# Kernel tuning notes

Measured on AMD Instinct MI355X. Metric: run time of the kernel, lower is better.

Reference implementation:

```python
import jax, jax.numpy as jnp
import numpy as np

N_NODES = 100000
N_EDGES = 1200000
N_GRAPHS = 256
D_IN = 8
D_H = 64


def setup_inputs() -> dict:
    key = jax.random.key(0)
    ks = jax.random.split(key, 16)
    x = jax.random.normal(ks[0], (N_NODES, D_IN), dtype=jnp.float32)
    edge_index = jax.random.randint(ks[1], (2, N_EDGES), 0, N_NODES, dtype=jnp.int64)
    batch = jnp.sort(jax.random.randint(ks[2], (N_NODES,), 0, N_GRAPHS, dtype=jnp.int64))

    def lin(k, fan_in, fan_out):
        s = 1.0 / np.sqrt(fan_in)
        return jax.random.uniform(k, (fan_in, fan_out), jnp.float32, -s, s)

    # SAGEConv: lin_l (aggregated neighbors, has bias), lin_r (root, no bias)
    W1l = lin(ks[3], D_IN, D_H); b1 = jnp.zeros((D_H,), jnp.float32); W1r = lin(ks[4], D_IN, D_H)
    W2l = lin(ks[5], D_H, D_H);  b2 = jnp.zeros((D_H,), jnp.float32); W2r = lin(ks[6], D_H, D_H)
    W3l = lin(ks[7], D_H, D_H);  b3 = jnp.zeros((D_H,), jnp.float32); W3r = lin(ks[8], D_H, D_H)
    Wc1 = lin(ks[9], D_H, D_H // 2); bc1 = jnp.zeros((D_H // 2,), jnp.float32)
    Wc2 = lin(ks[10], D_H // 2, 1);  bc2 = jnp.zeros((1,), jnp.float32)
    return dict(x=x, edge_index=edge_index, batch=batch,
                W1l=W1l, b1=b1, W1r=W1r, W2l=W2l, b2=b2, W2r=W2r,
                W3l=W3l, b3=b3, W3r=W3r, Wc1=Wc1, bc1=bc1, Wc2=Wc2, bc2=bc2)


def _sage_conv(x, src, dst, Wl, b, Wr):
    # mean-aggregate messages from source -> target, then two linears
    msg = x[src]                                             # [E, d] gather
    agg = jax.ops.segment_sum(msg, dst, num_segments=N_NODES)
    cnt = jax.ops.segment_sum(jnp.ones((src.shape[0],), x.dtype), dst,
                              num_segments=N_NODES)
    mean = agg / jnp.maximum(cnt, 1.0)[:, None]
    return mean @ Wl + b + x @ Wr


def reference(x, edge_index, batch, W1l, b1, W1r, W2l, b2, W2r,
              W3l, b3, W3r, Wc1, bc1, Wc2, bc2):
    src, dst = edge_index[0], edge_index[1]
    h = jax.nn.relu(_sage_conv(x, src, dst, W1l, b1, W1r))
    h = jax.nn.relu(_sage_conv(h, src, dst, W2l, b2, W2r))
    h = _sage_conv(h, src, dst, W3l, b3, W3r)
    g = jax.ops.segment_sum(h, batch, num_segments=N_GRAPHS)  # global_add_pool
    # dropout is identity in eval mode
    g = jax.nn.relu(g @ Wc1 + bc1)
    return g @ Wc2 + bc2
```

## Files before the change

kernel.cpp:

```cpp
#include <hip/hip_runtime.h>

#define N_NODES 100000
#define N_EDGES 1200000
#define N_GRAPHS 256
#define NBUCK 392
#define EBLK 98
#define EPB 12245
#define DCAP 4608

typedef __attribute__((ext_vector_type(8))) short bf16x8;
typedef __attribute__((ext_vector_type(4))) float f32x4;

__device__ inline unsigned short f2b(float f) {
    union { float f; unsigned u; } c; c.f = f;
    unsigned u = c.u;
    u += 0x7fff + ((u >> 16) & 1);
    return (unsigned short)(u >> 16);
}
__device__ inline float blo(unsigned u) { union { unsigned i; float f; } c; c.i = u << 16; return c.f; }
__device__ inline float bhi(unsigned u) { union { unsigned i; float f; } c; c.i = u & 0xffff0000u; return c.f; }
__device__ inline float b2f(unsigned short h) { union { unsigned i; float f; } c; c.i = ((unsigned)h) << 16; return c.f; }

__global__ __launch_bounds__(256) void bucketA(const int* __restrict__ ei, int* __restrict__ histm) {
    __shared__ int h[NBUCK];
    int k = blockIdx.x, tid = threadIdx.x;
    for (int t = tid; t < NBUCK; t += 256) h[t] = 0;
    __syncthreads();
    int e0 = k * EPB, e1 = min(e0 + EPB, N_EDGES);
    for (int e = e0 + tid; e < e1; e += 256) {
        int dd = ei[N_EDGES + e];
        atomicAdd(&h[dd >> 8], 1);
    }
    __syncthreads();
    for (int t = tid; t < NBUCK; t += 256) histm[t * EBLK + k] = h[t];
}

__global__ __launch_bounds__(512) void bucketB(int* __restrict__ histm, int* __restrict__ bstart) {
    __shared__ int sb[512];
    int tid = threadIdx.x;
    int tot = 0;
    if (tid < NBUCK) {
        for (int k = 0; k < EBLK; k++) tot += histm[tid * EBLK + k];
    }
    sb[tid] = tot;
    __syncthreads();
    int acc = tot;
    for (int off = 1; off < 512; off <<= 1) {
        int v = (tid >= off) ? sb[tid - off] : 0;
        __syncthreads();
        sb[tid] = acc = acc + v;
        __syncthreads();
    }
    int excl = acc - tot;
    if (tid < NBUCK) {
        bstart[tid] = excl;
        int run = excl;
        for (int k = 0; k < EBLK; k++) {
            int v = histm[tid * EBLK + k];
            histm[tid * EBLK + k] = run;
            run += v;
        }
    }
    if (tid == 0) bstart[NBUCK] = N_EDGES;
}

__global__ __launch_bounds__(256) void bucketC(const int* __restrict__ ei, const int* __restrict__ histm,
                                               int* __restrict__ ebuf) {
    __shared__ int cur[NBUCK];
    int k = blockIdx.x, tid = threadIdx.x;
    for (int t = tid; t < NBUCK; t += 256) cur[t] = histm[t * EBLK + k];
    __syncthreads();
    int e0 = k * EPB, e1 = min(e0 + EPB, N_EDGES);
    for (int e = e0 + tid; e < e1; e += 256) {
        int ss = ei[e];
        int dd = ei[N_EDGES + e];
        int pos = atomicAdd(&cur[dd >> 8], 1);
        ebuf[pos] = (ss << 8) | (dd & 255);
    }
}

__global__ __launch_bounds__(256) void bucketD(const int* __restrict__ ebuf, const int* __restrict__ bstart,
                                               int* __restrict__ rowptr, int* __restrict__ esrc) {
    __shared__ int ecache[DCAP];
    __shared__ int stage[DCAP];
    __shared__ int hist[256], off[256];
    int b = blockIdx.x, tid = threadIdx.x;
    int seg0 = bstart[b], seg1 = bstart[b + 1];
    int cnt = seg1 - seg0;
    hist[tid] = 0;
    int lim = min(cnt, DCAP);
    for (int i = tid; i < lim; i += 256) ecache[i] = ebuf[seg0 + i];
    __syncthreads();
    for (int i = tid; i < cnt; i += 256) {
        int p = (i < DCAP) ? ecache[i] : ebuf[seg0 + i];
        atomicAdd(&hist[p & 255], 1);
    }
    __syncthreads();
    int v = hist[tid];
    off[tid] = v;
    __syncthreads();
    int acc = v;
    for (int o = 1; o < 256; o <<= 1) {
        int t = (tid >= o) ? off[tid - o] : 0;
        __syncthreads();
        off[tid] = acc = acc + t;
        __syncthreads();
    }
    int excl = acc - v;
    rowptr[b * 256 + tid] = seg0 + excl;
    off[tid] = excl;
    __syncthreads();
    if (cnt <= DCAP) {
        for (int i = tid; i < cnt; i += 256) {
            int p = ecache[i];
            int pos = atomicAdd(&off[p & 255], 1);
            stage[pos] = (p >> 8) << 7;
        }
        __syncthreads();
        for (int i = tid; i < cnt; i += 256) esrc[seg0 + i] = stage[i];
    } else {
        for (int i = tid; i < cnt; i += 256) {
            int p = (i < DCAP) ? ecache[i] : ebuf[seg0 + i];
            int pos = atomicAdd(&off[p & 255], 1);
            esrc[seg0 + pos] = (p >> 8) << 7;
        }
    }
}

__global__ __launch_bounds__(256) void setup_kernel(const float* __restrict__ x, unsigned short* __restrict__ xb,
                                                    const float* __restrict__ W2l, const float* __restrict__ W2r,
                                                    unsigned short* __restrict__ pw2, float* __restrict__ zbase) {
    int blk = blockIdx.x, tid = threadIdx.x;
    if (blk < 391) {
        int n = blk * 256 + tid;
        if (n < N_NODES) {
            const float4* x4 = (const float4*)x;
            float4 v0 = x4[(size_t)n * 2], v1 = x4[(size_t)n * 2 + 1];
            uint4 p;
            p.x = (unsigned)f2b(v0.x) | ((unsigned)f2b(v0.y) << 16);
            p.y = (unsigned)f2b(v0.z) | ((unsigned)f2b(v0.w) << 16);
            p.z = (unsigned)f2b(v1.x) | ((unsigned)f2b(v1.y) << 16);
            p.w = (unsigned)f2b(v1.z) | ((unsigned)f2b(v1.w) << 16);
            ((uint4*)xb)[n] = p;
        }
    } else if (blk < 423) {
        int r = (blk - 391) * 256 + tid;
        int j = r & 7, lane = (r >> 3) & 63, t = (r >> 9) & 3, s = (r >> 11) & 3;
        int k = s * 32 + (lane >> 4) * 8 + j;
        int n = t * 16 + (lane & 15);
        float v = (k < 64) ? W2l[k * 64 + n] : W2r[(k - 64) * 64 + n];
        pw2[r] = f2b(v);
    } else {
        int i = (blk - 423) * 256 + tid;
        if (i < 33024) zbase[i] = 0.0f;
    }
}

__global__ __launch_bounds__(256) void layer1_fused(const float* __restrict__ x, const unsigned short* __restrict__ xb,
                                                    const int* __restrict__ rowptr, const int* __restrict__ esrc,
                                                    const float* __restrict__ Wl, const float* __restrict__ b,
                                                    const float* __restrict__ Wr, unsigned short* __restrict__ ob) {
    __shared__ float sa[4][8], sx[4][8];
    int tid = threadIdx.x;
    int sub = tid >> 6, lane = tid & 63;
    int grp = lane >> 2, q = lane & 3;
    int n = blockIdx.x * 4 + sub;
    int r0 = __builtin_amdgcn_readfirstlane(rowptr[n]);
    int r1 = __builtin_amdgcn_readfirstlane(rowptr[n + 1]);
    const unsigned* xbu = (const unsigned*)xb;
    float a0 = 0.f, a1 = 0.f;
#pragma unroll
    for (int c = 0; c < 2; c++) {
        int idx = r0 + 16 * c + grp;
        if (idx < r1) {
            unsigned v = xbu[(esrc[idx] >> 5) + q];
            a0 += blo(v); a1 += bhi(v);
        }
    }
    for (int e = r0 + 32; e < r1; e += 16) {
        int idx = e + grp;
        if (idx < r1) {
            unsigned v = xbu[(esrc[idx] >> 5) + q];
            a0 += blo(v); a1 += bhi(v);
        }
    }
#pragma unroll
    for (int m = 4; m <= 32; m <<= 1) {
        a0 += __shfl_xor(a0, m);
        a1 += __shfl_xor(a1, m);
    }
    if (lane < 4) { sa[sub][2 * lane] = a0; sa[sub][2 * lane + 1] = a1; }
    if (lane >= 8 && lane < 16) sx[sub][lane - 8] = x[(size_t)n * 8 + (lane - 8)];
    __syncthreads();
    float invn = 1.0f / fmaxf((float)(r1 - r0), 1.0f);
    float al = 0.f, ar = 0.f;
#pragma unroll
    for (int kk = 0; kk < 8; kk++) {
        al += sa[sub][kk] * Wl[kk * 64 + lane];
        ar += sx[sub][kk] * Wr[kk * 64 + lane];
    }
    ob[(size_t)n * 64 + lane] = f2b(fmaxf(al * invn + b[lane] + ar, 0.0f));
}

__global__ __launch_bounds__(256) void agg_gemm(const unsigned short* __restrict__ hb,
                                                const int* __restrict__ rowptr,
                                                const int* __restrict__ esrc,
                                                const unsigned short* __restrict__ pw,
                                                const float* __restrict__ bias,
                                                unsigned short* __restrict__ outb) {
    __shared__ unsigned short smean[16][64];
    int tid = threadIdx.x;
    int sub = tid >> 6, lane = tid & 63;
    int grp = lane >> 3, q = lane & 7;
    int tile = blockIdx.x;
    const uint4* h16 = (const uint4*)hb;
    for (int i = 0; i < 4; i++) {
        int n = tile * 16 + sub * 4 + i;
        int r0 = __builtin_amdgcn_readfirstlane(rowptr[n]);
        int r1 = __builtin_amdgcn_readfirstlane(rowptr[n + 1]);
        uint4 v[3];
#pragma unroll
        for (int c = 0; c < 3; c++) {
            uint4 vv; vv.x = 0u; vv.y = 0u; vv.z = 0u; vv.w = 0u;
            int idx = r0 + 8 * c + grp;
            if (idx < r1) vv = h16[(esrc[idx] >> 4) + q];
            v[c] = vv;
        }
        float a[8];
#pragma unroll
        for (int j = 0; j < 8; j++) a[j] = 0.f;
#pragma unroll
        for (int c = 0; c < 3; c++) {
            a[0] += blo(v[c].x); a[1] += bhi(v[c].x);
            a[2] += blo(v[c].y); a[3] += bhi(v[c].y);
            a[4] += blo(v[c].z); a[5] += bhi(v[c].z);
            a[6] += blo(v[c].w); a[7] += bhi(v[c].w);
        }
        for (int e = r0 + 24; e < r1; e += 8) {
            int idx = e + grp;
            if (idx < r1) {
                uint4 vv = h16[(esrc[idx] >> 4) + q];
                a[0] += blo(vv.x); a[1] += bhi(vv.x);
                a[2] += blo(vv.y); a[3] += bhi(vv.y);
                a[4] += blo(vv.z); a[5] += bhi(vv.z);
                a[6] += blo(vv.w); a[7] += bhi(vv.w);
            }
        }
#pragma unroll
        for (int j = 0; j < 8; j++) {
            a[j] += __shfl_xor(a[j], 8);
            a[j] += __shfl_xor(a[j], 16);
            a[j] += __shfl_xor(a[j], 32);
        }
        if (grp == 0) {
            float invn = 1.0f / fmaxf((float)(r1 - r0), 1.0f);
#pragma unroll
            for (int j = 0; j < 8; j++) smean[sub * 4 + i][q * 8 + j] = f2b(a[j] * invn);
        }
    }
    __syncthreads();
    int col = lane & 15, quad = lane >> 4;
    int m = tile * 16 + col;
    union U { uint4 u; bf16x8 b; };
    U a0, a1, a2, a3;
    a0.u = *(const uint4*)&smean[col][quad * 8];
    a1.u = *(const uint4*)&smean[col][32 + quad * 8];
    const uint4* srow = (const uint4*)(hb + (size_t)m * 64);
    a2.u = srow[quad];
    a3.u = srow[4 + quad];
    const uint4* pwv = (const uint4*)pw;
    int t = sub;
    U b0, b1, b2, b3;
    b0.u = pwv[(0 * 4 + t) * 64 + lane];
    b1.u = pwv[(1 * 4 + t) * 64 + lane];
    b2.u = pwv[(2 * 4 + t) * 64 + lane];
    b3.u = pwv[(3 * 4 + t) * 64 + lane];
    f32x4 acc = {0.f, 0.f, 0.f, 0.f};
    acc = __builtin_amdgcn_mfma_f32_16x16x32_bf16(a0.b, b0.b, acc, 0, 0, 0);
    acc = __builtin_amdgcn_mfma_f32_16x16x32_bf16(a1.b, b1.b, acc, 0, 0, 0);
    acc = __builtin_amdgcn_mfma_f32_16x16x32_bf16(a2.b, b2.b, acc, 0, 0, 0);
    acc = __builtin_amdgcn_mfma_f32_16x16x32_bf16(a3.b, b3.b, acc, 0, 0, 0);
    float bi = bias[t * 16 + col];
#pragma unroll
    for (int i = 0; i < 4; i++) {
        int node = tile * 16 + quad * 4 + i;
        outb[(size_t)node * 64 + t * 16 + col] = f2b(fmaxf(acc[i] + bi, 0.0f));
    }
}

__global__ __launch_bounds__(256) void aggpool3(const unsigned short* __restrict__ hb,
                                                const int* __restrict__ rowptr,
                                                const int* __restrict__ esrc,
                                                const int* __restrict__ batch, float* __restrict__ A) {
    __shared__ float sa[4][64];
    __shared__ int sbat[4];
    int tid = threadIdx.x;
    int sub = tid >> 6, lane = tid & 63;
    int grp = lane >> 3, q = lane & 7;
    int n = blockIdx.x * 4 + sub;
    int r0 = __builtin_amdgcn_readfirstlane(rowptr[n]);
    int r1 = __builtin_amdgcn_readfirstlane(rowptr[n + 1]);
    const uint4* h16 = (const uint4*)hb;
    uint4 v[3];
#pragma unroll
    for (int c = 0; c < 3; c++) {
        uint4 vv; vv.x = 0u; vv.y = 0u; vv.z = 0u; vv.w = 0u;
        int idx = r0 + 8 * c + grp;
        if (idx < r1) {
            int off = esrc[idx];
            vv = h16[(off >> 4) + q];
        }
        v[c] = vv;
    }
    float a[8];
#pragma unroll
    for (int j = 0; j < 8; j++) a[j] = 0.f;
#pragma unroll
    for (int c = 0; c < 3; c++) {
        a[0] += blo(v[c].x); a[1] += bhi(v[c].x);
        a[2] += blo(v[c].y); a[3] += bhi(v[c].y);
        a[4] += blo(v[c].z); a[5] += bhi(v[c].z);
        a[6] += blo(v[c].w); a[7] += bhi(v[c].w);
    }
    for (int e = r0 + 24; e < r1; e += 8) {
        int idx = e + grp;
        if (idx < r1) {
            int off = esrc[idx];
            uint4 vv = h16[(off >> 4) + q];
            a[0] += blo(vv.x); a[1] += bhi(vv.x);
            a[2] += blo(vv.y); a[3] += bhi(vv.y);
            a[4] += blo(vv.z); a[5] += bhi(vv.z);
            a[6] += blo(vv.w); a[7] += bhi(vv.w);
        }
    }
#pragma unroll
    for (int j = 0; j < 8; j++) {
        a[j] += __shfl_xor(a[j], 8);
        a[j] += __shfl_xor(a[j], 16);
        a[j] += __shfl_xor(a[j], 32);
    }
    if (lane == 0) sbat[sub] = batch[n];
    if (grp == 0) {
        float invn = 1.0f / fmaxf((float)(r1 - r0), 1.0f);
#pragma unroll
        for (int j = 0; j < 8; j++) sa[sub][q * 8 + j] = a[j] * invn;
    }
    __syncthreads();
    if (sub == 0) {
        int b0 = sbat[0], b3v = sbat[3];
        if (b0 == b3v) {
            float s = sa[0][lane] + sa[1][lane] + sa[2][lane] + sa[3][lane];
            atomicAdd(&A[b0 * 64 + lane], s);
        } else {
            float acc = sa[0][lane]; int cur = b0;
#pragma unroll
            for (int i = 1; i < 4; i++) {
                int bi = sbat[i];
                if (bi != cur) { atomicAdd(&A[cur * 64 + lane], acc); cur = bi; acc = 0.f; }
                acc += sa[i][lane];
            }
            atomicAdd(&A[cur * 64 + lane], acc);
        }
    }
}

__global__ __launch_bounds__(256) void poolB_kernel(const unsigned short* __restrict__ hb,
                                                    const int* __restrict__ batch,
                                                    float* __restrict__ B, float* __restrict__ cntf) {
    int d = threadIdx.x & 63;
    int grp = threadIdx.x >> 6;
    int n0 = blockIdx.x * 256;
    int cur = -1; float acc = 0.f; int ac = 0;
    for (int i = grp; i < 256; i += 4) {
        int n = n0 + i;
        if (n >= N_NODES) break;
        int bb = batch[n];
        if (bb != cur) {
            if (cur >= 0) {
                atomicAdd(&B[cur * 64 + d], acc);
                if (d == 0) atomicAdd(&cntf[cur], (float)ac);
            }
            cur = bb; acc = 0.f; ac = 0;
        }
        acc += b2f(hb[(size_t)n * 64 + d]);
        ac++;
    }
    if (cur >= 0) {
        atomicAdd(&B[cur * 64 + d], acc);
        if (d == 0) atomicAdd(&cntf[cur], (float)ac);
    }
}

__global__ __launch_bounds__(256) void head2_kernel(const float* __restrict__ A, const float* __restrict__ B,
                                                    const float* __restrict__ cntf,
                                                    const float* __restrict__ W3l, const float* __restrict__ b3,
                                                    const float* __restrict__ W3r,
                                                    const float* __restrict__ Wc1, const float* __restrict__ bc1,
                                                    const float* __restrict__ Wc2, const float* __restrict__ bc2,
                                                    float* __restrict__ out) {
    __shared__ float sA[4][64], sB[4][64], sh3[4][64];
    int tid = threadIdx.x, sub = tid >> 6, lane = tid & 63;
    int gid = blockIdx.x * 4 + sub;
    sA[sub][lane] = A[gid * 64 + lane];
    sB[sub][lane] = B[gid * 64 + lane];
    float cg = cntf[gid];
    __syncthreads();
    float v = cg * b3[lane];
#pragma unroll 8
    for (int k = 0; k < 64; k++) {
        v += sA[sub][k] * W3l[k * 64 + lane] + sB[sub][k] * W3r[k * 64 + lane];
    }
    sh3[sub][lane] = v;
    __syncthreads();
    int j = lane & 31, kh = lane >> 5;
    float a = 0.f;
#pragma unroll
    for (int kk = 0; kk < 32; kk++) {
        int k = kh * 32 + kk;
        a += sh3[sub][k] * Wc1[k * 32 + j];
    }
    a += __shfl_xor(a, 32);
    float contrib = (lane < 32) ? fmaxf(a + bc1[j], 0.0f) * Wc2[j] : 0.0f;
    contrib += __shfl_xor(contrib, 16);
    contrib += __shfl_xor(contrib, 8);
    contrib += __shfl_xor(contrib, 4);
    contrib += __shfl_xor(contrib, 2);
    contrib += __shfl_xor(contrib, 1);
    if (lane == 0) out[gid] = contrib + bc2[0];
}

extern "C" void kernel_launch(void* const* d_in, const int* in_sizes, int n_in,
                              void* d_out, int out_size, void* d_ws, size_t ws_size,
                              hipStream_t stream) {
    const float* x   = (const float*)d_in[0];
    const int*   ei  = (const int*)d_in[1];
    const int*   bat = (const int*)d_in[2];
    const float* W1l = (const float*)d_in[3];
    const float* b1  = (const float*)d_in[4];
    const float* W1r = (const float*)d_in[5];
    const float* W2l = (const float*)d_in[6];
    const float* b2  = (const float*)d_in[7];
    const float* W2r = (const float*)d_in[8];
    const float* W3l = (const float*)d_in[9];
    const float* b3  = (const float*)d_in[10];
    const float* W3r = (const float*)d_in[11];
    const float* Wc1 = (const float*)d_in[12];
    const float* bc1 = (const float*)d_in[13];
    const float* Wc2 = (const float*)d_in[14];
    const float* bc2 = (const float*)d_in[15];

    float* ws = (float*)d_ws;
    int*    rowptr = (int*)(ws);
    int*    esrc   = (int*)(ws + 100352);
    float*  A      = ws + 1300480;
    float*  B      = ws + 1316864;
    float*  cntf   = ws + 1333248;
    unsigned short* pw2 = (unsigned short*)(ws + 1333504);
    unsigned short* xb  = (unsigned short*)(ws + 1337600);
    unsigned short* hb1 = (unsigned short*)(ws + 1737728);
    unsigned short* hb2 = (unsigned short*)(ws + 4937728);
    int*    ebuf   = (int*)(ws + 8137728);
    int*    histm  = (int*)(ws + 9337728);
    int*    bstart = (int*)(ws + 9376144);

    bucketA<<<EBLK, 256, 0, stream>>>(ei, histm);
    bucketB<<<1, 512, 0, stream>>>(histm, bstart);
    bucketC<<<EBLK, 256, 0, stream>>>(ei, histm, ebuf);
    bucketD<<<NBUCK, 256, 0, stream>>>(ebuf, bstart, rowptr, esrc);
    setup_kernel<<<552, 256, 0, stream>>>(x, xb, W2l, W2r, pw2, A);

    layer1_fused<<<N_NODES / 4, 256, 0, stream>>>(x, xb, rowptr, esrc, W1l, b1, W1r, hb1);
    agg_gemm<<<N_NODES / 16, 256, 0, stream>>>(hb1, rowptr, esrc, pw2, b2, hb2);
    aggpool3<<<N_NODES / 4, 256, 0, stream>>>(hb2, rowptr, esrc, bat, A);
    poolB_kernel<<<(N_NODES + 255) / 256, 256, 0, stream>>>(hb2, bat, B, cntf);

    head2_kernel<<<N_GRAPHS / 4, 256, 0, stream>>>(A, B, cntf, W3l, b3, W3r, Wc1, bc1, Wc2, bc2,
                                                   (float*)d_out);
}
```

Measured before the change: 313.2 us.

## Fuse edge histogram into setup kernel and pool layer-2 outputs inside agg_gemm

The bucketA histogram pass moves into setup_kernel as extra blocks, so one launch does the cast, weight packing, zeroing and edge histogram. The histogram layout becomes block-major so writes are contiguous. The separate poolB kernel is removed: agg_gemm adds its ReLU outputs per graph into B with atomics, and head2 gets node counts per graph by binary search on the sorted batch array. This saves two launches and one re-read of hb2, at the cost of more atomics in agg_gemm and of relying on batch being sorted.

New measurement: 274.2 us. 12.4% less time.

```diff
diff --git a/kernel.cpp b/kernel.cpp
--- a/kernel.cpp
+++ b/kernel.cpp
@@ -21,115 +21,11 @@
 __device__ inline float bhi(unsigned u) { union { unsigned i; float f; } c; c.i = u & 0xffff0000u; return c.f; }
 __device__ inline float b2f(unsigned short h) { union { unsigned i; float f; } c; c.i = ((unsigned)h) << 16; return c.f; }
 
-__global__ __launch_bounds__(256) void bucketA(const int* __restrict__ ei, int* __restrict__ histm) {
-    __shared__ int h[NBUCK];
-    int k = blockIdx.x, tid = threadIdx.x;
-    for (int t = tid; t < NBUCK; t += 256) h[t] = 0;
-    __syncthreads();
-    int e0 = k * EPB, e1 = min(e0 + EPB, N_EDGES);
-    for (int e = e0 + tid; e < e1; e += 256) {
-        int dd = ei[N_EDGES + e];
-        atomicAdd(&h[dd >> 8], 1);
-    }
-    __syncthreads();
-    for (int t = tid; t < NBUCK; t += 256) histm[t * EBLK + k] = h[t];
-}
-
-__global__ __launch_bounds__(512) void bucketB(int* __restrict__ histm, int* __restrict__ bstart) {
-    __shared__ int sb[512];
-    int tid = threadIdx.x;
-    int tot = 0;
-    if (tid < NBUCK) {
-        for (int k = 0; k < EBLK; k++) tot += histm[tid * EBLK + k];
-    }
-    sb[tid] = tot;
-    __syncthreads();
-    int acc = tot;
-    for (int off = 1; off < 512; off <<= 1) {
-        int v = (tid >= off) ? sb[tid - off] : 0;
-        __syncthreads();
-        sb[tid] = acc = acc + v;
-        __syncthreads();
-    }
-    int excl = acc - tot;
-    if (tid < NBUCK) {
-        bstart[tid] = excl;
-        int run = excl;
-        for (int k = 0; k < EBLK; k++) {
-            int v = histm[tid * EBLK + k];
-            histm[tid * EBLK + k] = run;
-            run += v;
-        }
-    }
-    if (tid == 0) bstart[NBUCK] = N_EDGES;
-}
-
-__global__ __launch_bounds__(256) void bucketC(const int* __restrict__ ei, const int* __restrict__ histm,
-                                               int* __restrict__ ebuf) {
-    __shared__ int cur[NBUCK];
-    int k = blockIdx.x, tid = threadIdx.x;
-    for (int t = tid; t < NBUCK; t += 256) cur[t] = histm[t * EBLK + k];
-    __syncthreads();
-    int e0 = k * EPB, e1 = min(e0 + EPB, N_EDGES);
-    for (int e = e0 + tid; e < e1; e += 256) {
-        int ss = ei[e];
-        int dd = ei[N_EDGES + e];
-        int pos = atomicAdd(&cur[dd >> 8], 1);
-        ebuf[pos] = (ss << 8) | (dd & 255);
-    }
-}
-
-__global__ __launch_bounds__(256) void bucketD(const int* __restrict__ ebuf, const int* __restrict__ bstart,
-                                               int* __restrict__ rowptr, int* __restrict__ esrc) {
-    __shared__ int ecache[DCAP];
-    __shared__ int stage[DCAP];
-    __shared__ int hist[256], off[256];
-    int b = blockIdx.x, tid = threadIdx.x;
-    int seg0 = bstart[b], seg1 = bstart[b + 1];
-    int cnt = seg1 - seg0;
-    hist[tid] = 0;
-    int lim = min(cnt, DCAP);
-    for (int i = tid; i < lim; i += 256) ecache[i] = ebuf[seg0 + i];
-    __syncthreads();
-    for (int i = tid; i < cnt; i += 256) {
-        int p = (i < DCAP) ? ecache[i] : ebuf[seg0 + i];
-        atomicAdd(&hist[p & 255], 1);
-    }
-    __syncthreads();
-    int v = hist[tid];
-    off[tid] = v;
-    __syncthreads();
-    int acc = v;
-    for (int o = 1; o < 256; o <<= 1) {
-        int t = (tid >= o) ? off[tid - o] : 0;
-        __syncthreads();
-        off[tid] = acc = acc + t;
-        __syncthreads();
-    }
-    int excl = acc - v;
-    rowptr[b * 256 + tid] = seg0 + excl;
-    off[tid] = excl;
-    __syncthreads();
-    if (cnt <= DCAP) {
-        for (int i = tid; i < cnt; i += 256) {
-            int p = ecache[i];
-            int pos = atomicAdd(&off[p & 255], 1);
-            stage[pos] = (p >> 8) << 7;
-        }
-        __syncthreads();
-        for (int i = tid; i < cnt; i += 256) esrc[seg0 + i] = stage[i];
-    } else {
-        for (int i = tid; i < cnt; i += 256) {
-            int p = (i < DCAP) ? ecache[i] : ebuf[seg0 + i];
-            int pos = atomicAdd(&off[p & 255], 1);
-            esrc[seg0 + pos] = (p >> 8) << 7;
-        }
-    }
-}
-
 __global__ __launch_bounds__(256) void setup_kernel(const float* __restrict__ x, unsigned short* __restrict__ xb,
                                                     const float* __restrict__ W2l, const float* __restrict__ W2r,
-                                                    unsigned short* __restrict__ pw2, float* __restrict__ zbase) {
+                                                    unsigned short* __restrict__ pw2, float* __restrict__ zbase,
+                                                    const int* __restrict__ ei, int* __restrict__ histm) {
+    __shared__ int h[NBUCK];
     int blk = blockIdx.x, tid = threadIdx.x;
     if (blk < 391) {
         int n = blk * 256 + tid;
@@ -150,9 +46,112 @@
         int n = t * 16 + (lane & 15);
         float v = (k < 64) ? W2l[k * 64 + n] : W2r[(k - 64) * 64 + n];
         pw2[r] = f2b(v);
+    } else if (blk < 551) {
+        int i = (blk - 423) * 256 + tid;
+        zbase[i] = 0.0f;
     } else {
-        int i = (blk - 423) * 256 + tid;
-        if (i < 33024) zbase[i] = 0.0f;
+        int k = blk - 551;
+        for (int t = tid; t < NBUCK; t += 256) h[t] = 0;
+        __syncthreads();
+        int e0 = k * EPB, e1 = min(e0 + EPB, N_EDGES);
+        for (int e = e0 + tid; e < e1; e += 256) {
+            int dd = ei[N_EDGES + e];
+            atomicAdd(&h[dd >> 8], 1);
+        }
+        __syncthreads();
+        for (int t = tid; t < NBUCK; t += 256) histm[k * NBUCK + t] = h[t];
+    }
+}
+
+__global__ __launch_bounds__(512) void bucketB(int* __restrict__ histm, int* __restrict__ bstart) {
+    __shared__ int sb[512];
+    int tid = threadIdx.x;
+    int tot = 0;
+    if (tid < NBUCK) {
+        for (int k = 0; k < EBLK; k++) tot += histm[k * NBUCK + tid];
+    }
+    sb[tid] = tot;
+    __syncthreads();
+    int acc = tot;
+    for (int off = 1; off < 512; off <<= 1) {
+        int v = (tid >= off) ? sb[tid - off] : 0;
+        __syncthreads();
+        sb[tid] = acc = acc + v;
+        __syncthreads();
+    }
+    int excl = acc - tot;
+    if (tid < NBUCK) {
+        bstart[tid] = excl;
+        int run = excl;
+        for (int k = 0; k < EBLK; k++) {
+            int v = histm[k * NBUCK + tid];
+            histm[k * NBUCK + tid] = run;
+            run += v;
+        }
+    }
+    if (tid == 0) bstart[NBUCK] = N_EDGES;
+}
+
+__global__ __launch_bounds__(256) void bucketC(const int* __restrict__ ei, const int* __restrict__ histm,
+                                               int* __restrict__ ebuf) {
+    __shared__ int cur[NBUCK];
+    int k = blockIdx.x, tid = threadIdx.x;
+    for (int t = tid; t < NBUCK; t += 256) cur[t] = histm[k * NBUCK + t];
+    __syncthreads();
+    int e0 = k * EPB, e1 = min(e0 + EPB, N_EDGES);
+    for (int e = e0 + tid; e < e1; e += 256) {
+        int ss = ei[e];
+        int dd = ei[N_EDGES + e];
+        int pos = atomicAdd(&cur[dd >> 8], 1);
+        ebuf[pos] = (ss << 8) | (dd & 255);
+    }
+}
+
+__global__ __launch_bounds__(256) void bucketD(const int* __restrict__ ebuf, const int* __restrict__ bstart,
+                                               int* __restrict__ rowptr, int* __restrict__ esrc) {
+    __shared__ int ecache[DCAP];
+    __shared__ int stage[DCAP];
+    __shared__ int hist[256], off[256];
+    int b = blockIdx.x, tid = threadIdx.x;
+    int seg0 = bstart[b], seg1 = bstart[b + 1];
+    int cnt = seg1 - seg0;
+    hist[tid] = 0;
+    int lim = min(cnt, DCAP);
+    for (int i = tid; i < lim; i += 256) ecache[i] = ebuf[seg0 + i];
+    __syncthreads();
+    for (int i = tid; i < cnt; i += 256) {
+        int p = (i < DCAP) ? ecache[i] : ebuf[seg0 + i];
+        atomicAdd(&hist[p & 255], 1);
+    }
+    __syncthreads();
+    int v = hist[tid];
+    off[tid] = v;
+    __syncthreads();
+    int acc = v;
+    for (int o = 1; o < 256; o <<= 1) {
+        int t = (tid >= o) ? off[tid - o] : 0;
+        __syncthreads();
+        off[tid] = acc = acc + t;
+        __syncthreads();
+    }
+    int excl = acc - v;
+    rowptr[b * 256 + tid] = seg0 + excl;
+    off[tid] = excl;
+    __syncthreads();
+    if (cnt <= DCAP) {
+        for (int i = tid; i < cnt; i += 256) {
+            int p = ecache[i];
+            int pos = atomicAdd(&off[p & 255], 1);
+            stage[pos] = (p >> 8) << 7;
+        }
+        __syncthreads();
+        for (int i = tid; i < cnt; i += 256) esrc[seg0 + i] = stage[i];
+    } else {
+        for (int i = tid; i < cnt; i += 256) {
+            int p = (i < DCAP) ? ecache[i] : ebuf[seg0 + i];
+            int pos = atomicAdd(&off[p & 255], 1);
+            esrc[seg0 + pos] = (p >> 8) << 7;
+        }
     }
 }
 
@@ -207,13 +206,16 @@
                                                 const int* __restrict__ esrc,
                                                 const unsigned short* __restrict__ pw,
                                                 const float* __restrict__ bias,
-                                                unsigned short* __restrict__ outb) {
+                                                unsigned short* __restrict__ outb,
+                                                const int* __restrict__ batch, float* __restrict__ B) {
     __shared__ unsigned short smean[16][64];
+    __shared__ int sbat16[16];
     int tid = threadIdx.x;
     int sub = tid >> 6, lane = tid & 63;
     int grp = lane >> 3, q = lane & 7;
     int tile = blockIdx.x;
     const uint4* h16 = (const uint4*)hb;
+    if (tid < 16) sbat16[tid] = batch[tile * 16 + tid];
     for (int i = 0; i < 4; i++) {
         int n = tile * 16 + sub * 4 + i;
         int r0 = __builtin_amdgcn_readfirstlane(rowptr[n]);
@@ -281,10 +283,28 @@
     acc = __builtin_amdgcn_mfma_f32_16x16x32_bf16(a2.b, b2.b, acc, 0, 0, 0);
     acc = __builtin_amdgcn_mfma_f32_16x16x32_bf16(a3.b, b3.b, acc, 0, 0, 0);
     float bi = bias[t * 16 + col];
+    float v[4];
 #pragma unroll
     for (int i = 0; i < 4; i++) {
         int node = tile * 16 + quad * 4 + i;
-        outb[(size_t)node * 64 + t * 16 + col] = f2b(fmaxf(acc[i] + bi, 0.0f));
+        v[i] = fmaxf(acc[i] + bi, 0.0f);
+        outb[(size_t)node * 64 + t * 16 + col] = f2b(v[i]);
+    }
+    int g0 = sbat16[0], g15 = sbat16[15];
+    if (g0 == g15) {
+        float s = (v[0] + v[1]) + (v[2] + v[3]);
+        s += __shfl_xor(s, 16);
+        s += __shfl_xor(s, 32);
+        if (quad == 0) atomicAdd(&B[g0 * 64 + t * 16 + col], s);
+    } else {
+        float accp = 0.f; int cur = sbat16[quad * 4];
+#pragma unroll
+        for (int i = 0; i < 4; i++) {
+            int gi = sbat16[quad * 4 + i];
+            if (gi != cur) { atomicAdd(&B[cur * 64 + t * 16 + col], accp); cur = gi; accp = 0.f; }
+            accp += v[i];
+        }
+        atomicAdd(&B[cur * 64 + t * 16 + col], accp);
     }
 }
 
@@ -364,47 +384,28 @@
     }
 }
 
-__global__ __launch_bounds__(256) void poolB_kernel(const unsigned short* __restrict__ hb,
+__global__ __launch_bounds__(256) void head2_kernel(const float* __restrict__ A, const float* __restrict__ B,
                                                     const int* __restrict__ batch,
-                                                    float* __restrict__ B, float* __restrict__ cntf) {
-    int d = threadIdx.x & 63;
-    int grp = threadIdx.x >> 6;
-    int n0 = blockIdx.x * 256;
-    int cur = -1; float acc = 0.f; int ac = 0;
-    for (int i = grp; i < 256; i += 4) {
-        int n = n0 + i;
-        if (n >= N_NODES) break;
-        int bb = batch[n];
-        if (bb != cur) {
-            if (cur >= 0) {
-                atomicAdd(&B[cur * 64 + d], acc);
-                if (d == 0) atomicAdd(&cntf[cur], (float)ac);
-            }
-            cur = bb; acc = 0.f; ac = 0;
-        }
-        acc += b2f(hb[(size_t)n * 64 + d]);
-        ac++;
-    }
-    if (cur >= 0) {
-        atomicAdd(&B[cur * 64 + d], acc);
-        if (d == 0) atomicAdd(&cntf[cur], (float)ac);
-    }
-}
-
-__global__ __launch_bounds__(256) void head2_kernel(const float* __restrict__ A, const float* __restrict__ B,
-                                                    const float* __restrict__ cntf,
                                                     const float* __restrict__ W3l, const float* __restrict__ b3,
                                                     const float* __restrict__ W3r,
                                                     const float* __restrict__ Wc1, const float* __restrict__ bc1,
                                                     const float* __restrict__ Wc2, const float* __restrict__ bc2,
                                                     float* __restrict__ out) {
     __shared__ float sA[4][64], sB[4][64], sh3[4][64];
+    __shared__ float scnt[4];
     int tid = threadIdx.x, sub = tid >> 6, lane = tid & 63;
     int gid = blockIdx.x * 4 + sub;
     sA[sub][lane] = A[gid * 64 + lane];
     sB[sub][lane] = B[gid * 64 + lane];
-    float cg = cntf[gid];
-    __syncthreads();
+    if (lane == 0) {
+        int lo = 0, hi = N_NODES;
+        while (lo < hi) { int mid = (lo + hi) >> 1; if (batch[mid] < gid) lo = mid + 1; else hi = mid; }
+        int lo2 = lo, hi2 = N_NODES;
+        while (lo2 < hi2) { int mid = (lo2 + hi2) >> 1; if (batch[mid] < gid + 1) lo2 = mid + 1; else hi2 = mid; }
+        scnt[sub] = (float)(lo2 - lo);
+    }
+    __syncthreads();
+    float cg = scnt[sub];
     float v = cg * b3[lane];
 #pragma unroll 8
     for (int k = 0; k < 64; k++) {
@@ -454,7 +455,6 @@
     int*    esrc   = (int*)(ws + 100352);
     float*  A      = ws + 1300480;
     float*  B      = ws + 1316864;
-    float*  cntf   = ws + 1333248;
     unsigned short* pw2 = (unsigned short*)(ws + 1333504);
     unsigned short* xb  = (unsigned short*)(ws + 1337600);
     unsigned short* hb1 = (unsigned short*)(ws + 1737728);
@@ -463,17 +463,15 @@
     int*    histm  = (int*)(ws + 9337728);
     int*    bstart = (int*)(ws + 9376144);
 
-    bucketA<<<EBLK, 256, 0, stream>>>(ei, histm);
+    setup_kernel<<<649, 256, 0, stream>>>(x, xb, W2l, W2r, pw2, A, ei, histm);
     bucketB<<<1, 512, 0, stream>>>(histm, bstart);
     bucketC<<<EBLK, 256, 0, stream>>>(ei, histm, ebuf);
     bucketD<<<NBUCK, 256, 0, stream>>>(ebuf, bstart, rowptr, esrc);
-    setup_kernel<<<552, 256, 0, stream>>>(x, xb, W2l, W2r, pw2, A);
 
     layer1_fused<<<N_NODES / 4, 256, 0, stream>>>(x, xb, rowptr, esrc, W1l, b1, W1r, hb1);
-    agg_gemm<<<N_NODES / 16, 256, 0, stream>>>(hb1, rowptr, esrc, pw2, b2, hb2);
+    agg_gemm<<<N_NODES / 16, 256, 0, stream>>>(hb1, rowptr, esrc, pw2, b2, hb2, bat, B);
     aggpool3<<<N_NODES / 4, 256, 0, stream>>>(hb2, rowptr, esrc, bat, A);
-    poolB_kernel<<<(N_NODES + 255) / 256, 256, 0, stream>>>(hb2, bat, B, cntf);
-
-    head2_kernel<<<N_GRAPHS / 4, 256, 0, stream>>>(A, B, cntf, W3l, b3, W3r, Wc1, bc1, Wc2, bc2,
+
+    head2_kernel<<<N_GRAPHS / 4, 256, 0, stream>>>(A, B, bat, W3l, b3, W3r, Wc1, bc1, Wc2, bc2,
                                                    (float*)d_out);
 }
```
